# Kernel tuning notes

Hardware: AMD Instinct MI355X
Metric: run time of the kernel (lower is better)

Reference implementation:

```python
import jax, jax.numpy as jnp
import numpy as np

B, F, H, C = 256, 512, 1024, 1000
LN_EPS = 1e-5


def _proj(x, W, b, g, be):
    # AdaptiveAvgPool2d(1) + Flatten + Linear + LayerNorm + GELU(exact)
    p = x.mean(axis=(2, 3))                       # [B, Cin]
    h = p @ W + b                                 # [B, F]
    mu = h.mean(axis=-1, keepdims=True)
    var = h.var(axis=-1, keepdims=True)           # ddof=0, matches torch LayerNorm
    h = (h - mu) / jnp.sqrt(var + LN_EPS) * g + be
    return jax.nn.gelu(h, approximate=False)


def setup_inputs() -> dict:
    key = jax.random.key(0)
    ks = iter(jax.random.split(key, 64))
    def rn(shape, s=1.0):
        return jax.random.normal(next(ks), shape, jnp.float32) * s
    inp = {}
    feats = {"s1": (16, 112), "s2": (24, 56), "s3": (40, 28), "s4": (80, 14), "s5": (160, 7)}
    for n, (c, hw) in feats.items():
        inp[n] = rn((B, c, hw, hw))
    inp["ff"] = rn((B, 960, 7, 7))
    for i, c in enumerate([16, 24, 40, 80, 160], start=1):
        inp[f"Wp{i}"] = rn((c, F), 0.02)
        inp[f"bp{i}"] = jnp.zeros((F,), jnp.float32)
        inp[f"g{i}"] = jnp.ones((F,), jnp.float32)
        inp[f"be{i}"] = jnp.zeros((F,), jnp.float32)
    inp["Wg1"] = rn((960, H), 0.02); inp["bg1"] = jnp.zeros((H,), jnp.float32)
    inp["Wg2"] = rn((H, H // 2), 0.02); inp["bg2"] = jnp.zeros((H // 2,), jnp.float32)
    inp["Wg3"] = rn((H // 2, 5), 0.02); inp["bg3"] = jnp.zeros((5,), jnp.float32)
    inp["Wc1"] = rn((F, H), 0.02); inp["bc1"] = jnp.zeros((H,), jnp.float32)
    inp["Wc2"] = rn((H, H // 2), 0.02); inp["bc2"] = jnp.zeros((H // 2,), jnp.float32)
    inp["Wc3"] = rn((H // 2, C), 0.02); inp["bc3"] = jnp.zeros((C,), jnp.float32)
    return inp


def reference(s1, s2, s3, s4, s5, ff,
              Wp1, bp1, g1, be1, Wp2, bp2, g2, be2, Wp3, bp3, g3, be3,
              Wp4, bp4, g4, be4, Wp5, bp5, g5, be5,
              Wg1, bg1, Wg2, bg2, Wg3, bg3,
              Wc1, bc1, Wc2, bc2, Wc3, bc3):
    # gate on pooled final backbone features (dropout inactive at eval)
    gate_in = ff.mean(axis=(2, 3))                         # [B, 960]
    h = jax.nn.relu(gate_in @ Wg1 + bg1)
    h = jax.nn.relu(h @ Wg2 + bg2)
    gate_logits = h @ Wg3 + bg3                            # [B, 5]

    # per-stage projections -> [B, 5, F]
    stack = jnp.stack([
        _proj(s1, Wp1, bp1, g1, be1),
        _proj(s2, Wp2, bp2, g2, be2),
        _proj(s3, Wp3, bp3, g3, be3),
        _proj(s4, Wp4, bp4, g4, be4),
        _proj(s5, Wp5, bp5, g5, be5),
    ], axis=1)

    topv, topi = jax.lax.top_k(gate_logits, 2)             # [B, 2]
    w = jax.nn.softmax(topv, axis=1)                       # softmax over top-k logits
    sel = jnp.take_along_axis(stack, topi[:, :, None], axis=1)  # [B, 2, F]
    mixture = (sel * w[:, :, None]).sum(axis=1)            # [B, F]

    h = jax.nn.relu(mixture @ Wc1 + bc1)
    h = jax.nn.relu(h @ Wc2 + bc2)
    logits = h @ Wc3 + bc3                                 # [B, C]
    return logits, gate_logits, topi, w
```

## Files before the change

kernel.cpp:

```cpp
#include <hip/hip_runtime.h>
#include <math.h>


struct Pool4Segs {
    const float* src[4];
    float*       dst[4];
    int n4[4];
    int cum[4];
    float inv[4];
};

__global__ __launch_bounds__(256) void pool_big_kernel(Pool4Segs S, int total_waves) {
    int gid  = blockIdx.x * 256 + threadIdx.x;
    int wave = gid >> 6;
    int lane = gid & 63;
    if (wave >= total_waves) return;
    int s = 0;
    #pragma unroll
    for (int i = 0; i < 3; ++i) if (wave >= S.cum[i]) s = i + 1;
    int row = wave - (s == 0 ? 0 : S.cum[s - 1]);
    const int n4 = S.n4[s];
    const float4* p4 = (const float4*)(S.src[s]) + (size_t)row * n4;

    float a0 = 0.f, a1 = 0.f, a2 = 0.f, a3 = 0.f;
    float a4 = 0.f, a5 = 0.f, a6 = 0.f, a7 = 0.f;
    int k = lane;
    for (; k + 448 < n4; k += 512) {
        float4 v0 = p4[k];       float4 v1 = p4[k + 64];
        float4 v2 = p4[k + 128]; float4 v3 = p4[k + 192];
        float4 v4 = p4[k + 256]; float4 v5 = p4[k + 320];
        float4 v6 = p4[k + 384]; float4 v7 = p4[k + 448];
        a0 += (v0.x + v0.y) + (v0.z + v0.w);
        a1 += (v1.x + v1.y) + (v1.z + v1.w);
        a2 += (v2.x + v2.y) + (v2.z + v2.w);
        a3 += (v3.x + v3.y) + (v3.z + v3.w);
        a4 += (v4.x + v4.y) + (v4.z + v4.w);
        a5 += (v5.x + v5.y) + (v5.z + v5.w);
        a6 += (v6.x + v6.y) + (v6.z + v6.w);
        a7 += (v7.x + v7.y) + (v7.z + v7.w);
    }
    for (; k + 192 < n4; k += 256) {
        float4 v0 = p4[k];       float4 v1 = p4[k + 64];
        float4 v2 = p4[k + 128]; float4 v3 = p4[k + 192];
        a0 += (v0.x + v0.y) + (v0.z + v0.w);
        a1 += (v1.x + v1.y) + (v1.z + v1.w);
        a2 += (v2.x + v2.y) + (v2.z + v2.w);
        a3 += (v3.x + v3.y) + (v3.z + v3.w);
    }
    for (; k < n4; k += 64) {
        float4 v = p4[k];
        a0 += (v.x + v.y) + (v.z + v.w);
    }
    float acc = ((a0 + a1) + (a2 + a3)) + ((a4 + a5) + (a6 + a7));
    #pragma unroll
    for (int off = 32; off > 0; off >>= 1) acc += __shfl_down(acc, off, 64);
    if (lane == 0) S.dst[s][row] = acc * S.inv[s];
}

__global__ __launch_bounds__(256) void pool_small_kernel(const float* __restrict__ s5,
        const float* __restrict__ ff, float* __restrict__ dst5, float* __restrict__ dstf,
        int rows5) {
    __shared__ float lds[64 * 49];
    const int tid  = threadIdx.x;
    const int row0 = blockIdx.x * 64;
    const float* src;
    float* dst;
    int rbase;
    if (row0 < rows5) { src = s5; dst = dst5; rbase = row0; }
    else              { src = ff; dst = dstf; rbase = row0 - rows5; }
    const float4* p4 = (const float4*)(src + (size_t)rbase * 49);
    float4* l4 = (float4*)lds;
    float4 v0 = p4[tid];
    float4 v1 = p4[tid + 256];
    float4 v2 = p4[tid + 512];
    float4 v3;
    const bool t3 = (tid < 784 - 768);
    if (t3) v3 = p4[tid + 768];
    l4[tid]       = v0;
    l4[tid + 256] = v1;
    l4[tid + 512] = v2;
    if (t3) l4[tid + 768] = v3;
    __syncthreads();
    const int r  = tid >> 2;
    const int c0 = tid & 3;
    float s = 0.f;
    #pragma unroll
    for (int c = c0; c < 49; c += 4) s += lds[r * 49 + c];
    s += __shfl_down(s, 2, 64);
    s += __shfl_down(s, 1, 64);
    if (c0 == 0) dst[rbase + r] = s * (1.f / 49.f);
}

__global__ __launch_bounds__(256) void fc_tile_kernel(const float* __restrict__ X,
        const float* __restrict__ W, float* __restrict__ P,
        int M, int K, int N, int Kc, int ntiles) {
    __shared__ __align__(16) float Xs[16][68];
    __shared__ __align__(16) float Ws[16][68];
    const int tpk = 4 * ntiles;
    int bid = blockIdx.x;
    int ks  = bid / tpk;
    int rem = bid - ks * tpk;
    int mt  = rem / ntiles;
    int nt  = rem - mt * ntiles;
    const int m0 = mt * 64, n0 = nt * 64;
    const int k0 = ks * Kc;
    int k1 = k0 + Kc; if (k1 > K) k1 = K;

    const int tid = threadIdx.x;
    const int tm = tid & 15;
    const int tn = tid >> 4;
    const int xr = tid >> 2, xc = tid & 3;
    const int wr = tid >> 4, wc = tid & 15;
    const int nwc = n0 + wc * 4;

    float4 acc[4];
    #pragma unroll
    for (int r = 0; r < 4; ++r) acc[r] = make_float4(0.f, 0.f, 0.f, 0.f);

    float4 xv, wv;
    xv = *(const float4*)(X + (size_t)(m0 + xr) * K + k0 + xc * 4);
    if (nwc + 3 < N) {
        wv = *(const float4*)(W + (size_t)(k0 + wr) * N + nwc);
    } else {
        wv.x = (nwc + 0 < N) ? W[(size_t)(k0 + wr) * N + nwc + 0] : 0.f;
        wv.y = (nwc + 1 < N) ? W[(size_t)(k0 + wr) * N + nwc + 1] : 0.f;
        wv.z = (nwc + 2 < N) ? W[(size_t)(k0 + wr) * N + nwc + 2] : 0.f;
        wv.w = (nwc + 3 < N) ? W[(size_t)(k0 + wr) * N + nwc + 3] : 0.f;
    }

    for (int kt = k0; kt < k1; kt += 16) {
        __syncthreads();
        Xs[xc * 4 + 0][xr] = xv.x;
        Xs[xc * 4 + 1][xr] = xv.y;
        Xs[xc * 4 + 2][xr] = xv.z;
        Xs[xc * 4 + 3][xr] = xv.w;
        *(float4*)&Ws[wr][wc * 4] = wv;
        __syncthreads();
        if (kt + 16 < k1) {
            xv = *(const float4*)(X + (size_t)(m0 + xr) * K + kt + 16 + xc * 4);
            if (nwc + 3 < N) {
                wv = *(const float4*)(W + (size_t)(kt + 16 + wr) * N + nwc);
            } else {
                wv.x = (nwc + 0 < N) ? W[(size_t)(kt + 16 + wr) * N + nwc + 0] : 0.f;
                wv.y = (nwc + 1 < N) ? W[(size_t)(kt + 16 + wr) * N + nwc + 1] : 0.f;
                wv.z = (nwc + 2 < N) ? W[(size_t)(kt + 16 + wr) * N + nwc + 2] : 0.f;
                wv.w = (nwc + 3 < N) ? W[(size_t)(kt + 16 + wr) * N + nwc + 3] : 0.f;
            }
        }
        #pragma unroll
        for (int kk = 0; kk < 16; ++kk) {
            float4 xr4 = *(const float4*)&Xs[kk][tm * 4];
            float4 wr4 = *(const float4*)&Ws[kk][tn * 4];
            acc[0].x += xr4.x * wr4.x; acc[0].y += xr4.x * wr4.y;
            acc[0].z += xr4.x * wr4.z; acc[0].w += xr4.x * wr4.w;
            acc[1].x += xr4.y * wr4.x; acc[1].y += xr4.y * wr4.y;
            acc[1].z += xr4.y * wr4.z; acc[1].w += xr4.y * wr4.w;
            acc[2].x += xr4.z * wr4.x; acc[2].y += xr4.z * wr4.y;
            acc[2].z += xr4.z * wr4.z; acc[2].w += xr4.z * wr4.w;
            acc[3].x += xr4.w * wr4.x; acc[3].y += xr4.w * wr4.y;
            acc[3].z += xr4.w * wr4.z; acc[3].w += xr4.w * wr4.w;
        }
    }
    const int nbase = n0 + tn * 4;
    #pragma unroll
    for (int r = 0; r < 4; ++r) {
        int row = m0 + tm * 4 + r;
        float* pp = P + ((size_t)ks * M + row) * N + nbase;
        if (nbase + 3 < N) {
            *(float4*)pp = acc[r];
        } else {
            float v[4] = { acc[r].x, acc[r].y, acc[r].z, acc[r].w };
            for (int c = 0; c < 4; ++c) if (nbase + c < N) pp[c] = v[c];
        }
    }
}

__global__ __launch_bounds__(256) void reduce_bias_kernel(const float* __restrict__ P,
        const float* __restrict__ bias, float* __restrict__ Y,
        int MN, int N, int KS, int do_relu) {
    int i = (blockIdx.x * 256 + threadIdx.x) * 4;
    if (i >= MN) return;
    float4 a = *(const float4*)(P + i);
    for (int s = 1; s < KS; ++s) {
        float4 b = *(const float4*)(P + (size_t)s * MN + i);
        a.x += b.x; a.y += b.y; a.z += b.z; a.w += b.w;
    }
    int n = i - (i / N) * N;
    float4 bb = *(const float4*)(bias + n);
    a.x += bb.x; a.y += bb.y; a.z += bb.z; a.w += bb.w;
    if (do_relu) {
        a.x = fmaxf(a.x, 0.f); a.y = fmaxf(a.y, 0.f);
        a.z = fmaxf(a.z, 0.f); a.w = fmaxf(a.w, 0.f);
    }
    *(float4*)(Y + i) = a;
}

struct ProjParams {
    const float* W[5];
    const float* bp[5];
    const float* g[5];
    const float* be[5];
    int K[5];
    int poff[5];
};

__global__ __launch_bounds__(256) void proj_gemm_kernel(ProjParams P,
        const float* __restrict__ pools, float* __restrict__ proj_out) {
    __shared__ __align__(16) float Xs[8][68];
    __shared__ __align__(16) float Ws[8][68];
    const int st = blockIdx.y;
    const int K  = P.K[st];
    const float* X = pools + P.poff[st];
    const float* W = P.W[st];
    const int N = 512;
    int bid = blockIdx.x;
    int mt  = bid >> 3;
    int nt  = bid & 7;
    const int m0 = mt * 64, n0 = nt * 64;

    const int tid = threadIdx.x;
    const int tm = tid & 15;
    const int tn = tid >> 4;
    const int xa = tid >> 3, xb = tid & 7;
    const int wc = tid & 63, wb = tid >> 6;
    const int nw = n0 + wc;

    float4 acc[4];
    #pragma unroll
    for (int r = 0; r < 4; ++r) acc[r] = make_float4(0.f, 0.f, 0.f, 0.f);

    float x0, x1, w0v, w1v;
    x0  = X[(size_t)(m0 + xa) * K + xb];
    x1  = X[(size_t)(m0 + xa + 32) * K + xb];
    w0v = W[(size_t)wb * N + nw];
    w1v = W[(size_t)(wb + 4) * N + nw];

    for (int kt = 0; kt < K; kt += 8) {
        __syncthreads();
        Xs[xb][xa] = x0; Xs[xb][xa + 32] = x1;
        Ws[wb][wc] = w0v; Ws[wb + 4][wc] = w1v;
        __syncthreads();
        if (kt + 8 < K) {
            x0  = X[(size_t)(m0 + xa) * K + kt + 8 + xb];
            x1  = X[(size_t)(m0 + xa + 32) * K + kt + 8 + xb];
            w0v = W[(size_t)(kt + 8 + wb) * N + nw];
            w1v = W[(size_t)(kt + 8 + wb + 4) * N + nw];
        }
        #pragma unroll
        for (int kk = 0; kk < 8; ++kk) {
            float4 xr = *(const float4*)&Xs[kk][tm * 4];
            float4 wr = *(const float4*)&Ws[kk][tn * 4];
            acc[0].x += xr.x * wr.x; acc[0].y += xr.x * wr.y;
            acc[0].z += xr.x * wr.z; acc[0].w += xr.x * wr.w;
            acc[1].x += xr.y * wr.x; acc[1].y += xr.y * wr.y;
            acc[1].z += xr.y * wr.z; acc[1].w += xr.y * wr.w;
            acc[2].x += xr.z * wr.x; acc[2].y += xr.z * wr.y;
            acc[2].z += xr.z * wr.z; acc[2].w += xr.z * wr.w;
            acc[3].x += xr.w * wr.x; acc[3].y += xr.w * wr.y;
            acc[3].z += xr.w * wr.z; acc[3].w += xr.w * wr.w;
        }
    }
    const int nbase = n0 + tn * 4;
    float4 bb = *(const float4*)(P.bp[st] + nbase);
    float* op = proj_out + (size_t)st * 131072 + (size_t)(m0 + tm * 4) * N + nbase;
    #pragma unroll
    for (int r = 0; r < 4; ++r) {
        float4 v = acc[r];
        v.x += bb.x; v.y += bb.y; v.z += bb.z; v.w += bb.w;
        *(float4*)(op + (size_t)r * N) = v;
    }
}

__global__ __launch_bounds__(256) void fc3_top2_kernel(const float* __restrict__ X,
        const float* __restrict__ W, const float* __restrict__ bias,
        int* __restrict__ topi, float* __restrict__ wsm,
        float* __restrict__ out_gl, float* __restrict__ out_topi,
        float* __restrict__ out_w, int K) {
    const int b    = blockIdx.x;
    const int tid  = threadIdx.x;
    const int lane = tid & 63;
    const int wv   = tid >> 6;
    __shared__ float red[4][5];
    const float* x = X + (size_t)b * K;
    float acc[5] = {0.f, 0.f, 0.f, 0.f, 0.f};
    for (int k = tid; k < K; k += 256) {
        float xv = x[k];
        const float* wr = W + (size_t)k * 5;
        acc[0] += xv * wr[0]; acc[1] += xv * wr[1]; acc[2] += xv * wr[2];
        acc[3] += xv * wr[3]; acc[4] += xv * wr[4];
    }
    #pragma unroll
    for (int off = 32; off > 0; off >>= 1) {
        #pragma unroll
        for (int j = 0; j < 5; ++j) acc[j] += __shfl_down(acc[j], off, 64);
    }
    if (lane == 0) {
        #pragma unroll
        for (int j = 0; j < 5; ++j) red[wv][j] = acc[j];
    }
    __syncthreads();
    if (tid == 0) {
        float v[5];
        #pragma unroll
        for (int j = 0; j < 5; ++j)
            v[j] = ((red[0][j] + red[1][j]) + (red[2][j] + red[3][j])) + bias[j];
        int i0 = 0;
        #pragma unroll
        for (int i = 1; i < 5; ++i) if (v[i] > v[i0]) i0 = i;
        int i1 = -1;
        #pragma unroll
        for (int i = 0; i < 5; ++i) {
            if (i == i0) continue;
            if (i1 < 0 || v[i] > v[i1]) i1 = i;
        }
        float e1 = __expf(v[i1] - v[i0]);
        float inv = 1.f / (1.f + e1);
        float w0 = inv, w1 = e1 * inv;
        topi[b * 2] = i0; topi[b * 2 + 1] = i1;
        wsm[b * 2] = w0;  wsm[b * 2 + 1] = w1;
        #pragma unroll
        for (int j = 0; j < 5; ++j) out_gl[b * 5 + j] = v[j];
        out_topi[b * 2]     = (float)i0;
        out_topi[b * 2 + 1] = (float)i1;
        out_w[b * 2]     = w0;
        out_w[b * 2 + 1] = w1;
    }
}

__global__ __launch_bounds__(512) void mixln_kernel(ProjParams P,
        const float* __restrict__ proj_out, const int* __restrict__ topi,
        const float* __restrict__ wsm, float* __restrict__ mix) {
    const int b = blockIdx.x;
    const int f = threadIdx.x;
    __shared__ float redS[8], redQ[8];
    __shared__ float s_mu, s_rstd;

    float acc = 0.f;
    for (int j = 0; j < 2; ++j) {
        __syncthreads();
        const int st = topi[b * 2 + j];
        float h = proj_out[(size_t)st * 131072 + (size_t)b * 512 + f];

        float s = h, q = h * h;
        #pragma unroll
        for (int off = 32; off > 0; off >>= 1) {
            s += __shfl_down(s, off, 64);
            q += __shfl_down(q, off, 64);
        }
        const int lane = threadIdx.x & 63, wid = threadIdx.x >> 6;
        if (lane == 0) { redS[wid] = s; redQ[wid] = q; }
        __syncthreads();
        if (threadIdx.x == 0) {
            float ts = 0.f, tq = 0.f;
            #pragma unroll
            for (int i = 0; i < 8; ++i) { ts += redS[i]; tq += redQ[i]; }
            float mu  = ts * (1.f / 512.f);
            float var = tq * (1.f / 512.f) - mu * mu;
            s_mu   = mu;
            s_rstd = rsqrtf(var + 1e-5f);
        }
        __syncthreads();

        float x  = (h - s_mu) * s_rstd * P.g[st][f] + P.be[st][f];
        float ge = 0.5f * x * (1.f + erff(x * 0.70710678118654752f));
        acc += wsm[b * 2 + j] * ge;
    }
    mix[(size_t)b * 512 + f] = acc;
}

extern "C" void kernel_launch(void* const* d_in, const int* in_sizes, int n_in,
                              void* d_out, int out_size, void* d_ws, size_t ws_size,
                              hipStream_t stream) {
    const int B = 256, F = 512, H = 1024, C = 1000;

    const float* s1 = (const float*)d_in[0];
    const float* s2 = (const float*)d_in[1];
    const float* s3 = (const float*)d_in[2];
    const float* s4 = (const float*)d_in[3];
    const float* s5 = (const float*)d_in[4];
    const float* ff = (const float*)d_in[5];
    const float *Wp[5], *bp[5], *g[5], *be[5];
    for (int i = 0; i < 5; ++i) {
        Wp[i] = (const float*)d_in[6 + 4 * i];
        bp[i] = (const float*)d_in[7 + 4 * i];
        g[i]  = (const float*)d_in[8 + 4 * i];
        be[i] = (const float*)d_in[9 + 4 * i];
    }
    const float* Wg1 = (const float*)d_in[26]; const float* bg1 = (const float*)d_in[27];
    const float* Wg2 = (const float*)d_in[28]; const float* bg2 = (const float*)d_in[29];
    const float* Wg3 = (const float*)d_in[30]; const float* bg3 = (const float*)d_in[31];
    const float* Wc1 = (const float*)d_in[32]; const float* bc1 = (const float*)d_in[33];
    const float* Wc2 = (const float*)d_in[34]; const float* bc2 = (const float*)d_in[35];
    const float* Wc3 = (const float*)d_in[36]; const float* bc3 = (const float*)d_in[37];

    float* ws = (float*)d_ws;
    const int Ks[5]   = {16, 24, 40, 80, 160};
    const int poff[5] = {0, 4096, 10240, 20480, 40960};
    float* pools    = ws;
    float* gate_in  = ws + 81920;
    float* g1h      = ws + 327680;
    float* g2h      = ws + 589824;
    float* wsm      = ws + 722176;
    int*   topi     = (int*)(ws + 722688);
    float* mix      = ws + 723200;
    float* c1h      = ws + 854272;
    float* c2h      = ws + 1116416;
    float* proj_out = ws + 1247488;
    const size_t part_off = 1902848;
    float* partials = ws + part_off;

    float* out      = (float*)d_out;
    float* out_gl   = out + 256000;
    float* out_topi = out + 257280;
    float* out_w    = out + 257792;

    {
        Pool4Segs Sa;
        for (int i = 0; i < 4; ++i) {
            Sa.src[i] = s1; Sa.dst[i] = pools + poff[0];
            Sa.n4[i] = 112 * 112 / 4; Sa.cum[i] = B * 16; Sa.inv[i] = 1.f / (112 * 112);
        }
        int waves_a = B * 16;
        pool_big_kernel<<<(waves_a * 64 + 255) / 256, 256, 0, stream>>>(Sa, waves_a);

        Pool4Segs Sb;
        const float* srcs[3] = { s2, s3, s4 };
        float* dsts[3] = { pools + poff[1], pools + poff[2], pools + poff[3] };
        const int rls[3]  = { 56 * 56, 28 * 28, 14 * 14 };
        const int rows[3] = { B * 24, B * 40, B * 80 };
        int cum = 0;
        for (int i = 0; i < 3; ++i) {
            Sb.src[i] = srcs[i]; Sb.dst[i] = dsts[i]; Sb.n4[i] = rls[i] / 4;
            cum += rows[i]; Sb.cum[i] = cum; Sb.inv[i] = 1.f / rls[i];
        }
        Sb.src[3] = srcs[2]; Sb.dst[3] = dsts[2]; Sb.n4[3] = rls[2] / 4;
        Sb.cum[3] = cum; Sb.inv[3] = 1.f / rls[2];
        pool_big_kernel<<<(cum * 64 + 255) / 256, 256, 0, stream>>>(Sb, cum);
    }
    {
        int rows5 = B * 160;
        int total = rows5 + B * 960;
        pool_small_kernel<<<total / 64, 256, 0, stream>>>(s5, ff, pools + poff[4], gate_in, rows5);
    }

    auto fc = [&](const float* X, const float* W, const float* bias, float* Y,
                  int K, int N, int KSwant, int do_relu) {
        const int M = 256;
        int ntiles = (N + 63) / 64;
        size_t avail = ws_size / 4 > part_off ? ws_size / 4 - part_off : 0;
        int KSmax = (int)(avail / ((size_t)M * N));
        int KS = KSwant; if (KS > KSmax) KS = KSmax; if (KS < 1) KS = 1;
        int Kc = (((K + KS - 1) / KS) + 15) & ~15;
        KS = (K + Kc - 1) / Kc;
        int blocks = KS * 4 * ntiles;
        fc_tile_kernel<<<blocks, 256, 0, stream>>>(X, W, partials, M, K, N, Kc, ntiles);
        int MN = M * N;
        reduce_bias_kernel<<<(MN / 4 + 255) / 256, 256, 0, stream>>>(
            partials, bias, Y, MN, N, KS, do_relu);
    };

    fc(gate_in, Wg1, bg1, g1h, 960, H, 8, 1);
    fc(g1h, Wg2, bg2, g2h, H, H / 2, 16, 1);
    fc3_top2_kernel<<<B, 256, 0, stream>>>(g2h, Wg3, bg3, topi, wsm,
                                           out_gl, out_topi, out_w, H / 2);

    ProjParams P;
    for (int i = 0; i < 5; ++i) {
        P.W[i] = Wp[i]; P.bp[i] = bp[i]; P.g[i] = g[i]; P.be[i] = be[i];
        P.K[i] = Ks[i]; P.poff[i] = poff[i];
    }
    proj_gemm_kernel<<<dim3(32, 5), 256, 0, stream>>>(P, pools, proj_out);
    mixln_kernel<<<B, 512, 0, stream>>>(P, proj_out, topi, wsm, mix);

    fc(mix, Wc1, bc1, c1h, F, H, 8, 1);
    fc(c1h, Wc2, bc2, c2h, H, H / 2, 16, 1);
    fc(c2h, Wc3, bc3, out, H / 2, C, 8, 0);
}
```

Baseline: 571.9 us.

## Fuse split-K reductions into consumer GEMM loads and merge pooling launches

Removes the separate reduce_bias kernels: each split-K GEMM writes raw partial slabs, and the next layer sums the partials, adds bias and applies ReLU while loading its X tile (and the fc3/top2 kernel sums 16 partials directly). The final classifier layer runs without split-K and adds bias in its epilogue, writing straight to the output. The three pooling launches are merged into one kernel that dispatches big-spatial and small-spatial blocks by block index. This cuts kernel launches and intermediate round trips, but multiplies X-load traffic by the split count in consumer GEMMs and leaves the final layer with few blocks.

Measured after the change: 604.6 us. 1.06x slower.

```diff
diff --git a/kernel.cpp b/kernel.cpp
--- a/kernel.cpp
+++ b/kernel.cpp
@@ -2,72 +2,75 @@
 #include <math.h>
 
 
-struct Pool4Segs {
+struct PoolAll {
     const float* src[4];
     float*       dst[4];
     int n4[4];
     int cum[4];
     float inv[4];
+    const float* s5;
+    const float* ff;
+    float*       dst5;
+    float*       dstf;
+    int nbb;
+    int rows5;
 };
 
-__global__ __launch_bounds__(256) void pool_big_kernel(Pool4Segs S, int total_waves) {
-    int gid  = blockIdx.x * 256 + threadIdx.x;
-    int wave = gid >> 6;
-    int lane = gid & 63;
-    if (wave >= total_waves) return;
-    int s = 0;
-    #pragma unroll
-    for (int i = 0; i < 3; ++i) if (wave >= S.cum[i]) s = i + 1;
-    int row = wave - (s == 0 ? 0 : S.cum[s - 1]);
-    const int n4 = S.n4[s];
-    const float4* p4 = (const float4*)(S.src[s]) + (size_t)row * n4;
-
-    float a0 = 0.f, a1 = 0.f, a2 = 0.f, a3 = 0.f;
-    float a4 = 0.f, a5 = 0.f, a6 = 0.f, a7 = 0.f;
-    int k = lane;
-    for (; k + 448 < n4; k += 512) {
-        float4 v0 = p4[k];       float4 v1 = p4[k + 64];
-        float4 v2 = p4[k + 128]; float4 v3 = p4[k + 192];
-        float4 v4 = p4[k + 256]; float4 v5 = p4[k + 320];
-        float4 v6 = p4[k + 384]; float4 v7 = p4[k + 448];
-        a0 += (v0.x + v0.y) + (v0.z + v0.w);
-        a1 += (v1.x + v1.y) + (v1.z + v1.w);
-        a2 += (v2.x + v2.y) + (v2.z + v2.w);
-        a3 += (v3.x + v3.y) + (v3.z + v3.w);
-        a4 += (v4.x + v4.y) + (v4.z + v4.w);
-        a5 += (v5.x + v5.y) + (v5.z + v5.w);
-        a6 += (v6.x + v6.y) + (v6.z + v6.w);
-        a7 += (v7.x + v7.y) + (v7.z + v7.w);
-    }
-    for (; k + 192 < n4; k += 256) {
-        float4 v0 = p4[k];       float4 v1 = p4[k + 64];
-        float4 v2 = p4[k + 128]; float4 v3 = p4[k + 192];
-        a0 += (v0.x + v0.y) + (v0.z + v0.w);
-        a1 += (v1.x + v1.y) + (v1.z + v1.w);
-        a2 += (v2.x + v2.y) + (v2.z + v2.w);
-        a3 += (v3.x + v3.y) + (v3.z + v3.w);
-    }
-    for (; k < n4; k += 64) {
-        float4 v = p4[k];
-        a0 += (v.x + v.y) + (v.z + v.w);
-    }
-    float acc = ((a0 + a1) + (a2 + a3)) + ((a4 + a5) + (a6 + a7));
-    #pragma unroll
-    for (int off = 32; off > 0; off >>= 1) acc += __shfl_down(acc, off, 64);
-    if (lane == 0) S.dst[s][row] = acc * S.inv[s];
-}
-
-__global__ __launch_bounds__(256) void pool_small_kernel(const float* __restrict__ s5,
-        const float* __restrict__ ff, float* __restrict__ dst5, float* __restrict__ dstf,
-        int rows5) {
+__global__ __launch_bounds__(256) void pool_all_kernel(PoolAll S) {
     __shared__ float lds[64 * 49];
+    if ((int)blockIdx.x < S.nbb) {
+        int gid  = blockIdx.x * 256 + threadIdx.x;
+        int wave = gid >> 6;
+        int lane = gid & 63;
+        if (wave >= S.cum[3]) return;
+        int s = 0;
+        #pragma unroll
+        for (int i = 0; i < 3; ++i) if (wave >= S.cum[i]) s = i + 1;
+        int row = wave - (s == 0 ? 0 : S.cum[s - 1]);
+        const int n4 = S.n4[s];
+        const float4* p4 = (const float4*)(S.src[s]) + (size_t)row * n4;
+        float a0 = 0.f, a1 = 0.f, a2 = 0.f, a3 = 0.f;
+        float a4 = 0.f, a5 = 0.f, a6 = 0.f, a7 = 0.f;
+        int k = lane;
+        for (; k + 448 < n4; k += 512) {
+            float4 v0 = p4[k];       float4 v1 = p4[k + 64];
+            float4 v2 = p4[k + 128]; float4 v3 = p4[k + 192];
+            float4 v4 = p4[k + 256]; float4 v5 = p4[k + 320];
+            float4 v6 = p4[k + 384]; float4 v7 = p4[k + 448];
+            a0 += (v0.x + v0.y) + (v0.z + v0.w);
+            a1 += (v1.x + v1.y) + (v1.z + v1.w);
+            a2 += (v2.x + v2.y) + (v2.z + v2.w);
+            a3 += (v3.x + v3.y) + (v3.z + v3.w);
+            a4 += (v4.x + v4.y) + (v4.z + v4.w);
+            a5 += (v5.x + v5.y) + (v5.z + v5.w);
+            a6 += (v6.x + v6.y) + (v6.z + v6.w);
+            a7 += (v7.x + v7.y) + (v7.z + v7.w);
+        }
+        for (; k + 192 < n4; k += 256) {
+            float4 v0 = p4[k];       float4 v1 = p4[k + 64];
+            float4 v2 = p4[k + 128]; float4 v3 = p4[k + 192];
+            a0 += (v0.x + v0.y) + (v0.z + v0.w);
+            a1 += (v1.x + v1.y) + (v1.z + v1.w);
+            a2 += (v2.x + v2.y) + (v2.z + v2.w);
+            a3 += (v3.x + v3.y) + (v3.z + v3.w);
+        }
+        for (; k < n4; k += 64) {
+            float4 v = p4[k];
+            a0 += (v.x + v.y) + (v.z + v.w);
+        }
+        float acc = ((a0 + a1) + (a2 + a3)) + ((a4 + a5) + (a6 + a7));
+        #pragma unroll
+        for (int off = 32; off > 0; off >>= 1) acc += __shfl_down(acc, off, 64);
+        if (lane == 0) S.dst[s][row] = acc * S.inv[s];
+        return;
+    }
     const int tid  = threadIdx.x;
-    const int row0 = blockIdx.x * 64;
+    const int row0 = (blockIdx.x - S.nbb) * 64;
     const float* src;
     float* dst;
     int rbase;
-    if (row0 < rows5) { src = s5; dst = dst5; rbase = row0; }
-    else              { src = ff; dst = dstf; rbase = row0 - rows5; }
+    if (row0 < S.rows5) { src = S.s5; dst = S.dst5; rbase = row0; }
+    else                { src = S.ff; dst = S.dstf; rbase = row0 - S.rows5; }
     const float4* p4 = (const float4*)(src + (size_t)rbase * 49);
     float4* l4 = (float4*)lds;
     float4 v0 = p4[tid];
@@ -91,8 +94,10 @@
     if (c0 == 0) dst[rbase + r] = s * (1.f / 49.f);
 }
 
+template <int XKS, bool EPIB>
 __global__ __launch_bounds__(256) void fc_tile_kernel(const float* __restrict__ X,
-        const float* __restrict__ W, float* __restrict__ P,
+        const float* __restrict__ xbias, const float* __restrict__ W,
+        float* __restrict__ P, const float* __restrict__ bias,
         int M, int K, int N, int Kc, int ntiles) {
     __shared__ __align__(16) float Xs[16][68];
     __shared__ __align__(16) float Ws[16][68];
@@ -112,32 +117,58 @@
     const int xr = tid >> 2, xc = tid & 3;
     const int wr = tid >> 4, wc = tid & 15;
     const int nwc = n0 + wc * 4;
+    const size_t MK = (size_t)M * K;
+    const size_t xoff0 = (size_t)(m0 + xr) * K;
 
     float4 acc[4];
     #pragma unroll
     for (int r = 0; r < 4; ++r) acc[r] = make_float4(0.f, 0.f, 0.f, 0.f);
 
-    float4 xv, wv;
-    xv = *(const float4*)(X + (size_t)(m0 + xr) * K + k0 + xc * 4);
-    if (nwc + 3 < N) {
-        wv = *(const float4*)(W + (size_t)(k0 + wr) * N + nwc);
-    } else {
-        wv.x = (nwc + 0 < N) ? W[(size_t)(k0 + wr) * N + nwc + 0] : 0.f;
-        wv.y = (nwc + 1 < N) ? W[(size_t)(k0 + wr) * N + nwc + 1] : 0.f;
-        wv.z = (nwc + 2 < N) ? W[(size_t)(k0 + wr) * N + nwc + 2] : 0.f;
-        wv.w = (nwc + 3 < N) ? W[(size_t)(k0 + wr) * N + nwc + 3] : 0.f;
+    const int NXV = (XKS > 0) ? XKS : 1;
+    float4 xv[NXV];
+    float4 wv;
+
+    {
+        const size_t xo = xoff0 + k0 + xc * 4;
+        #pragma unroll
+        for (int ss = 0; ss < NXV; ++ss)
+            xv[ss] = *(const float4*)(X + (size_t)ss * MK + xo);
+        if (nwc + 3 < N) {
+            wv = *(const float4*)(W + (size_t)(k0 + wr) * N + nwc);
+        } else {
+            wv.x = (nwc + 0 < N) ? W[(size_t)(k0 + wr) * N + nwc + 0] : 0.f;
+            wv.y = (nwc + 1 < N) ? W[(size_t)(k0 + wr) * N + nwc + 1] : 0.f;
+            wv.z = (nwc + 2 < N) ? W[(size_t)(k0 + wr) * N + nwc + 2] : 0.f;
+            wv.w = (nwc + 3 < N) ? W[(size_t)(k0 + wr) * N + nwc + 3] : 0.f;
+        }
     }
 
     for (int kt = k0; kt < k1; kt += 16) {
         __syncthreads();
-        Xs[xc * 4 + 0][xr] = xv.x;
-        Xs[xc * 4 + 1][xr] = xv.y;
-        Xs[xc * 4 + 2][xr] = xv.z;
-        Xs[xc * 4 + 3][xr] = xv.w;
+        float4 xs = xv[0];
+        if (XKS > 0) {
+            #pragma unroll
+            for (int ss = 1; ss < NXV; ++ss) {
+                xs.x += xv[ss].x; xs.y += xv[ss].y;
+                xs.z += xv[ss].z; xs.w += xv[ss].w;
+            }
+            float4 xb = *(const float4*)(xbias + kt + xc * 4);
+            xs.x = fmaxf(xs.x + xb.x, 0.f);
+            xs.y = fmaxf(xs.y + xb.y, 0.f);
+            xs.z = fmaxf(xs.z + xb.z, 0.f);
+            xs.w = fmaxf(xs.w + xb.w, 0.f);
+        }
+        Xs[xc * 4 + 0][xr] = xs.x;
+        Xs[xc * 4 + 1][xr] = xs.y;
+        Xs[xc * 4 + 2][xr] = xs.z;
+        Xs[xc * 4 + 3][xr] = xs.w;
         *(float4*)&Ws[wr][wc * 4] = wv;
         __syncthreads();
         if (kt + 16 < k1) {
-            xv = *(const float4*)(X + (size_t)(m0 + xr) * K + kt + 16 + xc * 4);
+            const size_t xo = xoff0 + kt + 16 + xc * 4;
+            #pragma unroll
+            for (int ss = 0; ss < NXV; ++ss)
+                xv[ss] = *(const float4*)(X + (size_t)ss * MK + xo);
             if (nwc + 3 < N) {
                 wv = *(const float4*)(W + (size_t)(kt + 16 + wr) * N + nwc);
             } else {
@@ -166,33 +197,19 @@
     for (int r = 0; r < 4; ++r) {
         int row = m0 + tm * 4 + r;
         float* pp = P + ((size_t)ks * M + row) * N + nbase;
+        float4 v = acc[r];
+        if (EPIB && nbase + 3 < N) {
+            float4 bb = *(const float4*)(bias + nbase);
+            v.x += bb.x; v.y += bb.y; v.z += bb.z; v.w += bb.w;
+        }
         if (nbase + 3 < N) {
-            *(float4*)pp = acc[r];
+            *(float4*)pp = v;
         } else {
-            float v[4] = { acc[r].x, acc[r].y, acc[r].z, acc[r].w };
-            for (int c = 0; c < 4; ++c) if (nbase + c < N) pp[c] = v[c];
-        }
-    }
-}
-
-__global__ __launch_bounds__(256) void reduce_bias_kernel(const float* __restrict__ P,
-        const float* __restrict__ bias, float* __restrict__ Y,
-        int MN, int N, int KS, int do_relu) {
-    int i = (blockIdx.x * 256 + threadIdx.x) * 4;
-    if (i >= MN) return;
-    float4 a = *(const float4*)(P + i);
-    for (int s = 1; s < KS; ++s) {
-        float4 b = *(const float4*)(P + (size_t)s * MN + i);
-        a.x += b.x; a.y += b.y; a.z += b.z; a.w += b.w;
-    }
-    int n = i - (i / N) * N;
-    float4 bb = *(const float4*)(bias + n);
-    a.x += bb.x; a.y += bb.y; a.z += bb.z; a.w += bb.w;
-    if (do_relu) {
-        a.x = fmaxf(a.x, 0.f); a.y = fmaxf(a.y, 0.f);
-        a.z = fmaxf(a.z, 0.f); a.w = fmaxf(a.w, 0.f);
-    }
-    *(float4*)(Y + i) = a;
+            float vv[4] = { v.x, v.y, v.z, v.w };
+            for (int c = 0; c < 4; ++c)
+                if (nbase + c < N) pp[c] = vv[c] + (EPIB ? bias[nbase + c] : 0.f);
+        }
+    }
 }
 
 struct ProjParams {
@@ -271,20 +288,23 @@
     }
 }
 
-__global__ __launch_bounds__(256) void fc3_top2_kernel(const float* __restrict__ X,
-        const float* __restrict__ W, const float* __restrict__ bias,
-        int* __restrict__ topi, float* __restrict__ wsm,
-        float* __restrict__ out_gl, float* __restrict__ out_topi,
-        float* __restrict__ out_w, int K) {
+__global__ __launch_bounds__(256) void fc3_top2_kernel(const float* __restrict__ Xp,
+        const float* __restrict__ xbias, const float* __restrict__ W,
+        const float* __restrict__ bias, int* __restrict__ topi,
+        float* __restrict__ wsm, float* __restrict__ out_gl,
+        float* __restrict__ out_topi, float* __restrict__ out_w, int K) {
     const int b    = blockIdx.x;
     const int tid  = threadIdx.x;
     const int lane = tid & 63;
     const int wv   = tid >> 6;
     __shared__ float red[4][5];
-    const float* x = X + (size_t)b * K;
+    const size_t MK = (size_t)256 * K;
     float acc[5] = {0.f, 0.f, 0.f, 0.f, 0.f};
     for (int k = tid; k < K; k += 256) {
-        float xv = x[k];
+        float v = 0.f;
+        #pragma unroll
+        for (int s = 0; s < 16; ++s) v += Xp[(size_t)s * MK + (size_t)b * K + k];
+        float xv = fmaxf(v + xbias[k], 0.f);
         const float* wr = W + (size_t)k * 5;
         acc[0] += xv * wr[0]; acc[1] += xv * wr[1]; acc[2] += xv * wr[2];
         acc[3] += xv * wr[3]; acc[4] += xv * wr[4];
@@ -398,16 +418,12 @@
     const int poff[5] = {0, 4096, 10240, 20480, 40960};
     float* pools    = ws;
     float* gate_in  = ws + 81920;
-    float* g1h      = ws + 327680;
-    float* g2h      = ws + 589824;
-    float* wsm      = ws + 722176;
-    int*   topi     = (int*)(ws + 722688);
-    float* mix      = ws + 723200;
-    float* c1h      = ws + 854272;
-    float* c2h      = ws + 1116416;
-    float* proj_out = ws + 1247488;
-    const size_t part_off = 1902848;
-    float* partials = ws + part_off;
+    float* wsm      = ws + 327680;
+    int*   topi     = (int*)(ws + 328192);
+    float* mix      = ws + 328704;
+    float* proj_out = ws + 459776;
+    float* slabA    = ws + 1115136;
+    float* slabB    = ws + 3212288;
 
     float* out      = (float*)d_out;
     float* out_gl   = out + 256000;
@@ -415,53 +431,28 @@
     float* out_w    = out + 257792;
 
     {
-        Pool4Segs Sa;
+        PoolAll S;
+        const float* srcs[4] = { s1, s2, s3, s4 };
+        const int rls[4]  = { 112 * 112, 56 * 56, 28 * 28, 14 * 14 };
+        const int rows[4] = { B * 16, B * 24, B * 40, B * 80 };
+        int cum = 0;
         for (int i = 0; i < 4; ++i) {
-            Sa.src[i] = s1; Sa.dst[i] = pools + poff[0];
-            Sa.n4[i] = 112 * 112 / 4; Sa.cum[i] = B * 16; Sa.inv[i] = 1.f / (112 * 112);
-        }
-        int waves_a = B * 16;
-        pool_big_kernel<<<(waves_a * 64 + 255) / 256, 256, 0, stream>>>(Sa, waves_a);
-
-        Pool4Segs Sb;
-        const float* srcs[3] = { s2, s3, s4 };
-        float* dsts[3] = { pools + poff[1], pools + poff[2], pools + poff[3] };
-        const int rls[3]  = { 56 * 56, 28 * 28, 14 * 14 };
-        const int rows[3] = { B * 24, B * 40, B * 80 };
-        int cum = 0;
-        for (int i = 0; i < 3; ++i) {
-            Sb.src[i] = srcs[i]; Sb.dst[i] = dsts[i]; Sb.n4[i] = rls[i] / 4;
-            cum += rows[i]; Sb.cum[i] = cum; Sb.inv[i] = 1.f / rls[i];
-        }
-        Sb.src[3] = srcs[2]; Sb.dst[3] = dsts[2]; Sb.n4[3] = rls[2] / 4;
-        Sb.cum[3] = cum; Sb.inv[3] = 1.f / rls[2];
-        pool_big_kernel<<<(cum * 64 + 255) / 256, 256, 0, stream>>>(Sb, cum);
-    }
-    {
-        int rows5 = B * 160;
-        int total = rows5 + B * 960;
-        pool_small_kernel<<<total / 64, 256, 0, stream>>>(s5, ff, pools + poff[4], gate_in, rows5);
-    }
-
-    auto fc = [&](const float* X, const float* W, const float* bias, float* Y,
-                  int K, int N, int KSwant, int do_relu) {
-        const int M = 256;
-        int ntiles = (N + 63) / 64;
-        size_t avail = ws_size / 4 > part_off ? ws_size / 4 - part_off : 0;
-        int KSmax = (int)(avail / ((size_t)M * N));
-        int KS = KSwant; if (KS > KSmax) KS = KSmax; if (KS < 1) KS = 1;
-        int Kc = (((K + KS - 1) / KS) + 15) & ~15;
-        KS = (K + Kc - 1) / Kc;
-        int blocks = KS * 4 * ntiles;
-        fc_tile_kernel<<<blocks, 256, 0, stream>>>(X, W, partials, M, K, N, Kc, ntiles);
-        int MN = M * N;
-        reduce_bias_kernel<<<(MN / 4 + 255) / 256, 256, 0, stream>>>(
-            partials, bias, Y, MN, N, KS, do_relu);
-    };
-
-    fc(gate_in, Wg1, bg1, g1h, 960, H, 8, 1);
-    fc(g1h, Wg2, bg2, g2h, H, H / 2, 16, 1);
-    fc3_top2_kernel<<<B, 256, 0, stream>>>(g2h, Wg3, bg3, topi, wsm,
+            S.src[i] = srcs[i]; S.dst[i] = pools + poff[i]; S.n4[i] = rls[i] / 4;
+            cum += rows[i]; S.cum[i] = cum; S.inv[i] = 1.f / rls[i];
+        }
+        S.nbb   = (cum * 64) / 256;
+        S.s5    = s5; S.ff = ff;
+        S.dst5  = pools + poff[4]; S.dstf = gate_in;
+        S.rows5 = B * 160;
+        int small_blocks = (S.rows5 + B * 960) / 64;
+        pool_all_kernel<<<S.nbb + small_blocks, 256, 0, stream>>>(S);
+    }
+
+    fc_tile_kernel<0, false><<<8 * 4 * 16, 256, 0, stream>>>(
+        gate_in, nullptr, Wg1, slabA, nullptr, B, 960, H, 128, 16);
+    fc_tile_kernel<8, false><<<16 * 4 * 8, 256, 0, stream>>>(
+        slabA, bg1, Wg2, slabB, nullptr, B, H, H / 2, 64, 8);
+    fc3_top2_kernel<<<B, 256, 0, stream>>>(slabB, bg2, Wg3, bg3, topi, wsm,
                                            out_gl, out_topi, out_w, H / 2);
 
     ProjParams P;
@@ -472,7 +463,10 @@
     proj_gemm_kernel<<<dim3(32, 5), 256, 0, stream>>>(P, pools, proj_out);
     mixln_kernel<<<B, 512, 0, stream>>>(P, proj_out, topi, wsm, mix);
 
-    fc(mix, Wc1, bc1, c1h, F, H, 8, 1);
-    fc(c1h, Wc2, bc2, c2h, H, H / 2, 16, 1);
-    fc(c2h, Wc3, bc3, out, H / 2, C, 8, 0);
-}
+    fc_tile_kernel<0, false><<<8 * 4 * 16, 256, 0, stream>>>(
+        mix, nullptr, Wc1, slabA, nullptr, B, F, H, 64, 16);
+    fc_tile_kernel<8, false><<<16 * 4 * 8, 256, 0, stream>>>(
+        slabA, bc1, Wc2, slabB, nullptr, B, H, H / 2, 64, 8);
+    fc_tile_kernel<16, true><<<1 * 4 * 16, 256, 0, stream>>>(
+        slabB, bc2, Wc3, out, bc3, B, H / 2, C, 512, 16);
+}
```
